# Kernel optimization log

Measured on AMD Instinct MI355X. Metric: run time of the kernel, lower is better.

The kernel has to match this reference:

```python
import jax, jax.numpy as jnp
import numpy as np

MSE_W, SSIM_W = 0.6, 0.4
WIN, SIGMA = 11, 1.5


def _gaussian_window():
    coords = jnp.arange(WIN, dtype=jnp.float32) - (WIN - 1) / 2.0
    g = jnp.exp(-coords ** 2 / (2.0 * SIGMA ** 2))
    g = g / g.sum()
    w = jnp.outer(g, g)  # [11,11]
    return w.reshape(1, 1, WIN, WIN)  # OIHW


def _blur(x, window):
    # x: [B,1,H,W], valid conv with 11x11 gaussian
    return jax.lax.conv_general_dilated(
        x, window, window_strides=(1, 1), padding='VALID',
        dimension_numbers=('NCHW', 'OIHW', 'NCHW'))


def setup_inputs() -> dict:
    key = jax.random.key(0)
    k1, k2 = jax.random.split(key)
    pred = jax.random.uniform(k1, (32, 1, 512, 512), dtype=jnp.float32)
    target = jax.random.uniform(k2, (32, 1, 512, 512), dtype=jnp.float32)
    return {"pred": pred, "target": target}


def reference(pred, target):
    window = _gaussian_window()
    C1 = (0.01 * 1.0) ** 2
    C2 = (0.03 * 1.0) ** 2

    mse_loss = jnp.mean((pred - target) ** 2)

    mu1 = _blur(pred, window)
    mu2 = _blur(target, window)
    mu1_sq = mu1 * mu1
    mu2_sq = mu2 * mu2
    mu1_mu2 = mu1 * mu2
    sigma1_sq = _blur(pred * pred, window) - mu1_sq
    sigma2_sq = _blur(target * target, window) - mu2_sq
    sigma12 = _blur(pred * target, window) - mu1_mu2

    ssim_map = (2.0 * mu1_mu2 + C1) * (2.0 * sigma12 + C2) / (
        (mu1_sq + mu2_sq + C1) * (sigma1_sq + sigma2_sq + C2) + 1e-6)
    ssim_loss = 1.0 - jnp.mean(ssim_map)

    return MSE_W * mse_loss + SSIM_W * ssim_loss
```

## Files before the change

kernel.cpp:

```cpp
#include <hip/hip_runtime.h>
#include <math.h>

#define BATCH 32
#define H 512
#define W 512
#define OUT_HW 502
#define TS_X 32
#define BAND 48
#define NBANDS 3
#define STRIP (BAND * NBANDS)
#define RB_ROWS 58
#define RB_STRIDE 36
#define NTX 16
#define NSTRIP 4
#define NBLOCKS (NTX * NSTRIP * BATCH)
#define N1 ((double)BATCH * H * W)
#define N2 ((double)BATCH * OUT_HW * OUT_HW)

struct GaussW { float g[11]; };

__global__ __launch_bounds__(256, 2)
void ssim_strip_kernel(const float* __restrict__ pred,
                       const float* __restrict__ targ,
                       float* __restrict__ ws_contrib,
                       GaussW gw)
{
    __shared__ __align__(16) float rb[4][RB_ROWS * RB_STRIDE];
    __shared__ float red[8];

    const int tid = threadIdx.x;
    const int tx = blockIdx.x, sy = blockIdx.y, b = blockIdx.z;
    const int ox0 = tx * TS_X;
    const int S = sy * STRIP;
    const int cols = min(TS_X, OUT_HW - ox0);
    const int mse_end = S + STRIP;
    const bool interior_x = (ox0 + 44 <= W);

    const float* __restrict__ pb = pred + ((size_t)b << 18);
    const float* __restrict__ tb = targ + ((size_t)b << 18);

    const int br0 = 3 * (tid >> 4);
    const int bc0 = 2 * (tid & 15);

    float mse_local = 0.f, ssim_local = 0.f;

    #pragma unroll 1
    for (int band = 0; band < NBANDS; ++band) {
        const int out0 = S + band * BAND;
        if (out0 >= OUT_HW) break;
        const int brows = min(BAND, OUT_HW - out0);
        const int h0    = (band == 0) ? S : (out0 + 10);
        const int h1    = min(out0 + brows + 10, H);
        const int nnew  = h1 - h0;
        const int slot0 = h0 - out0;

        if (band > 0) {
            __syncthreads();
            if (tid < 80) {
                const int r = tid >> 3, q = (tid & 7) * 4;
                const int src = (BAND + r) * RB_STRIDE + q;
                const int dst = r * RB_STRIDE + q;
                float4 v0 = *(const float4*)&rb[0][src];
                float4 v1 = *(const float4*)&rb[1][src];
                float4 v2 = *(const float4*)&rb[2][src];
                float4 v3 = *(const float4*)&rb[3][src];
                *(float4*)&rb[0][dst] = v0;
                *(float4*)&rb[1][dst] = v1;
                *(float4*)&rb[2][dst] = v2;
                *(float4*)&rb[3][dst] = v3;
            }
            __syncthreads();
        }

        #pragma unroll 1
        for (int idx = tid; idx < nnew * 8; idx += 256) {
            const int r = idx >> 3, gq = idx & 7;
            const int c0 = 4 * gq;
            const int gy = h0 + r;
            const int base = (gy << 9) + ox0 + c0;
            float sv[16], dv[16], ss[16], dd[16];
            if (interior_x) {
                #pragma unroll
                for (int q = 0; q < 4; ++q) {
                    *(float4*)(sv + 4 * q) = *(const float4*)(pb + base + 4 * q);
                    *(float4*)(dv + 4 * q) = *(const float4*)(tb + base + 4 * q);
                }
            } else {
                #pragma unroll
                for (int q = 0; q < 4; ++q) {
                    int gx = ox0 + c0 + 4 * q;
                    float4 vp = make_float4(0.f, 0.f, 0.f, 0.f);
                    float4 vt = vp;
                    if (gx < W) {
                        vp = *(const float4*)(pb + base + 4 * q);
                        vt = *(const float4*)(tb + base + 4 * q);
                    }
                    *(float4*)(sv + 4 * q) = vp;
                    *(float4*)(dv + 4 * q) = vt;
                }
            }
            #pragma unroll
            for (int i = 0; i < 16; ++i) {
                float p = sv[i], t = dv[i];
                float s = p + t, d = p - t;
                sv[i] = s; dv[i] = d;
                ss[i] = s * s; dd[i] = d * d;
            }

            if (gy < mse_end)
                mse_local += dd[0] + dd[1] + dd[2] + dd[3];

            float a[4][4] = {};
            #pragma unroll
            for (int k = 0; k < 11; ++k) {
                float g = gw.g[k];
                #pragma unroll
                for (int j = 0; j < 4; ++j) {
                    a[0][j] = fmaf(g, sv[j + k], a[0][j]);
                    a[1][j] = fmaf(g, dv[j + k], a[1][j]);
                    a[2][j] = fmaf(g, ss[j + k], a[2][j]);
                    a[3][j] = fmaf(g, dd[j + k], a[3][j]);
                }
            }
            const int wr = (slot0 + r) * RB_STRIDE + c0;
            #pragma unroll
            for (int ch = 0; ch < 4; ++ch)
                *(float4*)(&rb[ch][wr]) = make_float4(a[ch][0], a[ch][1], a[ch][2], a[ch][3]);
        }
        __syncthreads();

        if (br0 < brows) {
            float acc[4][3][2] = {};
            #pragma unroll
            for (int jr = 0; jr < 13; ++jr) {
                int rr = br0 + jr;
                #pragma unroll
                for (int ch = 0; ch < 4; ++ch) {
                    float2 v = *(const float2*)(&rb[ch][rr * RB_STRIDE + bc0]);
                    #pragma unroll
                    for (int i = 0; i < 3; ++i) {
                        int k = jr - i;
                        if (k >= 0 && k < 11) {
                            float g = gw.g[k];
                            acc[ch][i][0] = fmaf(g, v.x, acc[ch][i][0]);
                            acc[ch][i][1] = fmaf(g, v.y, acc[ch][i][1]);
                        }
                    }
                }
            }
            const float C1 = 1e-4f, C2 = 9e-4f;
            #pragma unroll
            for (int i = 0; i < 3; ++i) {
                if (br0 + i < brows) {
                    #pragma unroll
                    for (int j = 0; j < 2; ++j) {
                        if (bc0 + j < cols) {
                            float A  = acc[0][i][j], Bv = acc[1][i][j];
                            float U  = acc[2][i][j], V  = acc[3][i][j];
                            float A2 = A * A, B2 = Bv * Bv;
                            float mu12_2 = 0.5f * (A2 - B2);
                            float musq   = 0.5f * (A2 + B2);
                            float sig12_2 = 0.5f * (U - V) - mu12_2;
                            float sigsum  = 0.5f * (U + V) - musq;
                            float num = (mu12_2 + C1) * (sig12_2 + C2);
                            float den = (musq + C1) * (sigsum + C2) + 1e-6f;
                            ssim_local += num / den;
                        }
                    }
                }
            }
        }
    }

    #pragma unroll
    for (int off = 32; off > 0; off >>= 1) {
        ssim_local += __shfl_down(ssim_local, off, 64);
        mse_local  += __shfl_down(mse_local,  off, 64);
    }
    int wave = tid >> 6;
    if ((tid & 63) == 0) { red[wave] = ssim_local; red[4 + wave] = mse_local; }
    __syncthreads();
    if (tid == 0) {
        float s = red[0] + red[1] + red[2] + red[3];
        float m = red[4] + red[5] + red[6] + red[7];
        double contrib = 0.6 * (double)m / N1 - 0.4 * (double)s / N2;
        int bid = (b * NSTRIP + sy) * NTX + tx;
        ws_contrib[bid] = (float)contrib;
    }
}

__global__ __launch_bounds__(1024)
void finalize_kernel(const float* __restrict__ ws_contrib,
                     float* __restrict__ out)
{
    __shared__ double rs[1024];
    int tid = threadIdx.x;
    double s = 0.0;
    for (int i = tid; i < NBLOCKS; i += 1024)
        s += (double)ws_contrib[i];
    rs[tid] = s;
    __syncthreads();
    for (int off = 512; off > 0; off >>= 1) {
        if (tid < off) rs[tid] += rs[tid + off];
        __syncthreads();
    }
    if (tid == 0)
        out[0] = (float)(0.4 + rs[0]);
}

extern "C" void kernel_launch(void* const* d_in, const int* in_sizes, int n_in,
                              void* d_out, int out_size, void* d_ws, size_t ws_size,
                              hipStream_t stream)
{
    const float* pred = (const float*)d_in[0];
    const float* targ = (const float*)d_in[1];
    float* out = (float*)d_out;
    float* ws_contrib = (float*)d_ws;

    GaussW gw;
    double g[11], sum = 0.0;
    for (int i = 0; i < 11; ++i) { double x = i - 5.0; g[i] = exp(-x * x / 4.5); sum += g[i]; }
    for (int i = 0; i < 11; ++i) gw.g[i] = (float)(g[i] / sum);

    ssim_strip_kernel<<<dim3(NTX, NSTRIP, BATCH), 256, 0, stream>>>(pred, targ, ws_contrib, gw);
    finalize_kernel<<<1, 1024, 0, stream>>>(ws_contrib, out);
}
```

Measured before the change: 125.3 us.

## Store row-blurred channels in fp16 and do vertical blur with packed half2 FMA

Stores the horizontally blurred intermediate channels in shared memory as half2, interleaving the four channels per column pair so one 16-byte load fetches all of them. The vertical blur then accumulates with packed __hfma2 instead of scalar fp32 FMAs. This halves LDS footprint and traffic and halves the vertical FMA count, which may allow more occupancy. The risk is precision: the variance terms come from subtracting squared means from blurred squares, so fp16 cancellation could push the SSIM result past tolerance.

```diff
diff --git a/kernel.cpp b/kernel.cpp
--- a/kernel.cpp
+++ b/kernel.cpp
@@ -1,4 +1,5 @@
 #include <hip/hip_runtime.h>
+#include <hip/hip_fp16.h>
 #include <math.h>
 
 #define BATCH 32
@@ -10,7 +11,6 @@
 #define NBANDS 3
 #define STRIP (BAND * NBANDS)
 #define RB_ROWS 58
-#define RB_STRIDE 36
 #define NTX 16
 #define NSTRIP 4
 #define NBLOCKS (NTX * NSTRIP * BATCH)
@@ -25,7 +25,7 @@
                        float* __restrict__ ws_contrib,
                        GaussW gw)
 {
-    __shared__ __align__(16) float rb[4][RB_ROWS * RB_STRIDE];
+    __shared__ __align__(16) __half2 rbh[RB_ROWS * 16 * 4];
     __shared__ float red[8];
 
     const int tid = threadIdx.x;
@@ -39,8 +39,13 @@
     const float* __restrict__ pb = pred + ((size_t)b << 18);
     const float* __restrict__ tb = targ + ((size_t)b << 18);
 
+    __half2 gh2[11];
+    #pragma unroll
+    for (int k = 0; k < 11; ++k) gh2[k] = __float2half2_rn(gw.g[k]);
+
     const int br0 = 3 * (tid >> 4);
-    const int bc0 = 2 * (tid & 15);
+    const int cp  = tid & 15;
+    const int bc0 = 2 * cp;
 
     float mse_local = 0.f, ssim_local = 0.f;
 
@@ -56,18 +61,10 @@
 
         if (band > 0) {
             __syncthreads();
-            if (tid < 80) {
-                const int r = tid >> 3, q = (tid & 7) * 4;
-                const int src = (BAND + r) * RB_STRIDE + q;
-                const int dst = r * RB_STRIDE + q;
-                float4 v0 = *(const float4*)&rb[0][src];
-                float4 v1 = *(const float4*)&rb[1][src];
-                float4 v2 = *(const float4*)&rb[2][src];
-                float4 v3 = *(const float4*)&rb[3][src];
-                *(float4*)&rb[0][dst] = v0;
-                *(float4*)&rb[1][dst] = v1;
-                *(float4*)&rb[2][dst] = v2;
-                *(float4*)&rb[3][dst] = v3;
+            if (tid < 160) {
+                const int r = tid >> 4, q = tid & 15;
+                *(float4*)&rbh[(r * 16 + q) * 4] =
+                    *(const float4*)&rbh[((BAND + r) * 16 + q) * 4];
             }
             __syncthreads();
         }
@@ -122,29 +119,37 @@
                     a[3][j] = fmaf(g, dd[j + k], a[3][j]);
                 }
             }
-            const int wr = (slot0 + r) * RB_STRIDE + c0;
-            #pragma unroll
-            for (int ch = 0; ch < 4; ++ch)
-                *(float4*)(&rb[ch][wr]) = make_float4(a[ch][0], a[ch][1], a[ch][2], a[ch][3]);
+            const int row = slot0 + r;
+            #pragma unroll
+            for (int cpl = 0; cpl < 2; ++cpl) {
+                __align__(16) __half2 hw[4];
+                #pragma unroll
+                for (int ch = 0; ch < 4; ++ch)
+                    hw[ch] = __floats2half2_rn(a[ch][2 * cpl], a[ch][2 * cpl + 1]);
+                *(float4*)&rbh[(row * 16 + (2 * gq + cpl)) * 4] = *(const float4*)hw;
+            }
         }
         __syncthreads();
 
         if (br0 < brows) {
-            float acc[4][3][2] = {};
+            __half2 acc[4][3];
+            #pragma unroll
+            for (int ch = 0; ch < 4; ++ch)
+                #pragma unroll
+                for (int i = 0; i < 3; ++i) acc[ch][i] = __float2half2_rn(0.f);
+
             #pragma unroll
             for (int jr = 0; jr < 13; ++jr) {
-                int rr = br0 + jr;
+                const int rr = br0 + jr;
+                __align__(16) __half2 hv[4];
+                *(float4*)hv = *(const float4*)&rbh[(rr * 16 + cp) * 4];
                 #pragma unroll
                 for (int ch = 0; ch < 4; ++ch) {
-                    float2 v = *(const float2*)(&rb[ch][rr * RB_STRIDE + bc0]);
                     #pragma unroll
                     for (int i = 0; i < 3; ++i) {
-                        int k = jr - i;
-                        if (k >= 0 && k < 11) {
-                            float g = gw.g[k];
-                            acc[ch][i][0] = fmaf(g, v.x, acc[ch][i][0]);
-                            acc[ch][i][1] = fmaf(g, v.y, acc[ch][i][1]);
-                        }
+                        const int k = jr - i;
+                        if (k >= 0 && k < 11)
+                            acc[ch][i] = __hfma2(gh2[k], hv[ch], acc[ch][i]);
                     }
                 }
             }
@@ -155,8 +160,14 @@
                     #pragma unroll
                     for (int j = 0; j < 2; ++j) {
                         if (bc0 + j < cols) {
-                            float A  = acc[0][i][j], Bv = acc[1][i][j];
-                            float U  = acc[2][i][j], V  = acc[3][i][j];
+                            float A, Bv, U, V;
+                            if (j == 0) {
+                                A = __low2float(acc[0][i]);  Bv = __low2float(acc[1][i]);
+                                U = __low2float(acc[2][i]);  V  = __low2float(acc[3][i]);
+                            } else {
+                                A = __high2float(acc[0][i]); Bv = __high2float(acc[1][i]);
+                                U = __high2float(acc[2][i]); V  = __high2float(acc[3][i]);
+                            }
                             float A2 = A * A, B2 = Bv * Bv;
                             float mu12_2 = 0.5f * (A2 - B2);
                             float musq   = 0.5f * (A2 + B2);
```

Measured after the change: 120.4 us. -3.9%, faster.
